# Kernel optimization log

Hardware: AMD Instinct MI355X
Metric: run time of the kernel (lower is better)

The kernel has to match this reference:

```python
import jax, jax.numpy as jnp
import numpy as np

SAMPLING_RATE = 0.5

def setup_inputs() -> dict:
    key = jax.random.key(0)
    k1, k2 = jax.random.split(key)
    token = jax.random.normal(k1, (8, 16, 4, 384), dtype=jnp.float32)
    feature = jax.random.normal(k2, (8, 16, 4, 196, 384), dtype=jnp.float32)
    return {"token": token, "feature": feature}

def reference(token, feature):
    b1, n1, kk1, c = token.shape
    b2, n2, kk2, hw, _ = feature.shape
    N = n1 * kk1  # == n2 * kk2
    tok = token.reshape(b1, N, 1, c)           # [b, N, 1, c]
    feat = feature.reshape(b2, N, hw, c)       # [b, N, hw, c]
    scale = c ** (-0.5)
    # attention scores: [b, N, 1, hw]
    attn = jnp.einsum('bnqc,bnhc->bnqh', tok, feat) * scale
    attn = jax.nn.softmax(attn, axis=-1)
    tk = int(hw * SAMPLING_RATE)
    sel_attn, sel_idx = jax.lax.top_k(attn, tk)          # [b, N, 1, tk]
    sel_attn = sel_attn / jnp.sum(sel_attn, axis=-1, keepdims=True)
    # gather selected features: idx [b, N, tk] -> feat rows [b, N, tk, c]
    idx = sel_idx[:, :, 0, :]                            # [b, N, tk]
    sel_feat = jnp.take_along_axis(feat, idx[..., None], axis=2)  # [b, N, tk, c]
    out = jnp.einsum('bnqt,bntc->bnqc', sel_attn, sel_feat)       # [b, N, 1, c]
    return out.reshape(b1, n1, kk1, c)
```

## Files before the change

### kernel.cpp

```cpp
#include <hip/hip_runtime.h>

#define HW 196
#define C  384
#define TK 98
#define NT 512
#define NWAVE (NT/64)
#define NQUAD ((HW+3)/4)

__global__ __launch_bounds__(NT) void sampling_kernel(
    const float* __restrict__ token,
    const float* __restrict__ feature,
    float* __restrict__ out)
{
    __shared__ float tokLds[C];
    __shared__ float score[HW];
    __shared__ float selW[TK];
    __shared__ int   selIdx[TK];
    __shared__ float wsum[NWAVE];
    __shared__ float part[NWAVE][C];
    __shared__ float s_max, s_winv;

    const int tid  = threadIdx.x;
    const int wave = tid >> 6;
    const int lane = tid & 63;
    const int pair = blockIdx.x;

    const float* tokp  = token   + (size_t)pair * C;
    const float* featp = feature + (size_t)pair * (HW * C);

    for (int i = tid; i < C; i += NT) tokLds[i] = tokp[i];
    __syncthreads();

    const float4* t4 = (const float4*)tokLds;
    float4 tb  = t4[lane];
    float4 tb2 = make_float4(0.f, 0.f, 0.f, 0.f);
    if (lane < 32) tb2 = t4[64 + lane];

    const float scale = 0.05103103630798288f;

    for (int q = wave; q < NQUAD; q += NWAVE) {
        const int rbase = q * 4;
        float4 a[4], b[4];
        #pragma unroll
        for (int j = 0; j < 4; ++j) {
            const float4* f4 = (const float4*)(featp + (rbase + j) * C);
            a[j] = f4[lane];
            if (lane < 32) b[j] = f4[64 + lane];
        }
        #pragma unroll
        for (int j = 0; j < 4; ++j) {
            float p = a[j].x*tb.x + a[j].y*tb.y + a[j].z*tb.z + a[j].w*tb.w;
            if (lane < 32)
                p += b[j].x*tb2.x + b[j].y*tb2.y + b[j].z*tb2.z + b[j].w*tb2.w;
            #pragma unroll
            for (int off = 32; off > 0; off >>= 1)
                p += __shfl_xor(p, off, 64);
            if (lane == 0) score[rbase + j] = p * scale;
        }
    }
    __syncthreads();

    if (wave == 0) {
        float m = -3.4e38f;
        for (int i = lane; i < HW; i += 64) m = fmaxf(m, score[i]);
        #pragma unroll
        for (int off = 32; off > 0; off >>= 1)
            m = fmaxf(m, __shfl_xor(m, off, 64));
        if (lane == 0) s_max = m;
    }
    __syncthreads();

    float w = 0.f;
    if (tid < HW) {
        const float si = score[tid];
        int rank = 0;
        for (int j = 0; j < HW; ++j) {
            const float sj = score[j];
            rank += (int)((sj > si) | ((sj == si) & (j < tid)));
        }
        if (rank < TK) {
            w = __expf(si - s_max);
            selIdx[rank] = tid;
            selW[rank]  = w;
        }
    }
    #pragma unroll
    for (int off = 32; off > 0; off >>= 1) w += __shfl_xor(w, off, 64);
    if (lane == 0) wsum[wave] = w;
    __syncthreads();
    if (tid == 0) {
        float s = 0.f;
        #pragma unroll
        for (int i = 0; i < NWAVE; ++i) s += wsum[i];
        s_winv = 1.f / s;
    }
    __syncthreads();

    float4 acc_a = make_float4(0.f, 0.f, 0.f, 0.f);
    float4 acc_b = make_float4(0.f, 0.f, 0.f, 0.f);
    for (int i = wave; i < TK; i += NWAVE) {
        const int   r   = selIdx[i];
        const float wgt = selW[i];
        const float4* f4 = (const float4*)(featp + (size_t)r * C);
        float4 a = f4[lane];
        acc_a.x += wgt * a.x; acc_a.y += wgt * a.y;
        acc_a.z += wgt * a.z; acc_a.w += wgt * a.w;
        if (lane < 32) {
            float4 b = f4[64 + lane];
            acc_b.x += wgt * b.x; acc_b.y += wgt * b.y;
            acc_b.z += wgt * b.z; acc_b.w += wgt * b.w;
        }
    }
    float4* pw = (float4*)&part[wave][0];
    pw[lane] = acc_a;
    if (lane < 32) pw[64 + lane] = acc_b;
    __syncthreads();

    if (tid < C) {
        float s = 0.f;
        #pragma unroll
        for (int wv = 0; wv < NWAVE; ++wv) s += part[wv][tid];
        out[(size_t)pair * C + tid] = s * s_winv;
    }
}

extern "C" void kernel_launch(void* const* d_in, const int* in_sizes, int n_in,
                              void* d_out, int out_size, void* d_ws, size_t ws_size,
                              hipStream_t stream) {
    const float* token   = (const float*)d_in[0];
    const float* feature = (const float*)d_in[1];
    float* out = (float*)d_out;
    const int pairs = in_sizes[0] / C;
    sampling_kernel<<<pairs, NT, 0, stream>>>(token, feature, out);
}
```

Measured before the change: 41.01 us.

## Split score rows across 4-lane groups and unroll gather loop by four

The score phase now gives each 4-lane group its own feature row, accumulating 24 float4 products per lane, so only two shuffle steps are needed per row instead of a full 64-lane reduction for every row. Token values are read from LDS inside the loop instead of being held in registers. The weighted-gather loop is unrolled by four so more row loads can be in flight at once. Launch bounds now request 4 blocks per CU. In the score phase each lane reads 16-byte chunks strided 64 bytes apart within a row, which is less contiguous per load instruction than before, and unrolling plus the occupancy hint may raise register pressure.

```diff
diff --git a/kernel.cpp b/kernel.cpp
--- a/kernel.cpp
+++ b/kernel.cpp
@@ -2,12 +2,12 @@
 
 #define HW 196
 #define C  384
+#define CF4 (C/4)
 #define TK 98
 #define NT 512
 #define NWAVE (NT/64)
-#define NQUAD ((HW+3)/4)
 
-__global__ __launch_bounds__(NT) void sampling_kernel(
+__global__ __launch_bounds__(NT, 4) void sampling_kernel(
     const float* __restrict__ token,
     const float* __restrict__ feature,
     float* __restrict__ out)
@@ -23,39 +23,37 @@
     const int tid  = threadIdx.x;
     const int wave = tid >> 6;
     const int lane = tid & 63;
+    const int g    = lane >> 2;
+    const int l    = lane & 3;
     const int pair = blockIdx.x;
 
     const float* tokp  = token   + (size_t)pair * C;
     const float* featp = feature + (size_t)pair * (HW * C);
+    const float4* f4base = (const float4*)featp;
+    const float4* t4     = (const float4*)tokLds;
 
     for (int i = tid; i < C; i += NT) tokLds[i] = tokp[i];
     __syncthreads();
 
-    const float4* t4 = (const float4*)tokLds;
-    float4 tb  = t4[lane];
-    float4 tb2 = make_float4(0.f, 0.f, 0.f, 0.f);
-    if (lane < 32) tb2 = t4[64 + lane];
-
     const float scale = 0.05103103630798288f;
 
-    for (int q = wave; q < NQUAD; q += NWAVE) {
-        const int rbase = q * 4;
-        float4 a[4], b[4];
-        #pragma unroll
-        for (int j = 0; j < 4; ++j) {
-            const float4* f4 = (const float4*)(featp + (rbase + j) * C);
-            a[j] = f4[lane];
-            if (lane < 32) b[j] = f4[64 + lane];
-        }
-        #pragma unroll
-        for (int j = 0; j < 4; ++j) {
-            float p = a[j].x*tb.x + a[j].y*tb.y + a[j].z*tb.z + a[j].w*tb.w;
-            if (lane < 32)
-                p += b[j].x*tb2.x + b[j].y*tb2.y + b[j].z*tb2.z + b[j].w*tb2.w;
+    #pragma unroll
+    for (int strip = 0; strip < 2; ++strip) {
+        const int r = strip * 128 + wave * 16 + g;
+        if (r < HW) {
+            const float4* f4 = f4base + (size_t)r * CF4;
+            float4 acc = make_float4(0.f, 0.f, 0.f, 0.f);
             #pragma unroll
-            for (int off = 32; off > 0; off >>= 1)
-                p += __shfl_xor(p, off, 64);
-            if (lane == 0) score[rbase + j] = p * scale;
+            for (int k = 0; k < 24; ++k) {
+                float4 a = f4[l + 4 * k];
+                float4 t = t4[l + 4 * k];
+                acc.x += a.x * t.x; acc.y += a.y * t.y;
+                acc.z += a.z * t.z; acc.w += a.w * t.w;
+            }
+            float s = (acc.x + acc.y) + (acc.z + acc.w);
+            s += __shfl_xor(s, 1, 64);
+            s += __shfl_xor(s, 2, 64);
+            if (l == 0) score[r] = s * scale;
         }
     }
     __syncthreads();
@@ -98,17 +96,23 @@
 
     float4 acc_a = make_float4(0.f, 0.f, 0.f, 0.f);
     float4 acc_b = make_float4(0.f, 0.f, 0.f, 0.f);
-    for (int i = wave; i < TK; i += NWAVE) {
-        const int   r   = selIdx[i];
-        const float wgt = selW[i];
-        const float4* f4 = (const float4*)(featp + (size_t)r * C);
-        float4 a = f4[lane];
-        acc_a.x += wgt * a.x; acc_a.y += wgt * a.y;
-        acc_a.z += wgt * a.z; acc_a.w += wgt * a.w;
-        if (lane < 32) {
-            float4 b = f4[64 + lane];
-            acc_b.x += wgt * b.x; acc_b.y += wgt * b.y;
-            acc_b.z += wgt * b.z; acc_b.w += wgt * b.w;
+    for (int base = wave; base < TK; base += 4 * NWAVE) {
+        #pragma unroll
+        for (int j = 0; j < 4; ++j) {
+            const int i = base + j * NWAVE;
+            if (i < TK) {
+                const int   r   = selIdx[i];
+                const float wgt = selW[i];
+                const float4* f4 = f4base + (size_t)r * CF4;
+                float4 a = f4[lane];
+                acc_a.x += wgt * a.x; acc_a.y += wgt * a.y;
+                acc_a.z += wgt * a.z; acc_a.w += wgt * a.w;
+                if (lane < 32) {
+                    float4 b = f4[64 + lane];
+                    acc_b.x += wgt * b.x; acc_b.y += wgt * b.y;
+                    acc_b.z += wgt * b.z; acc_b.w += wgt * b.w;
+                }
+            }
         }
     }
     float4* pw = (float4*)&part[wave][0];
```

New measurement: 39.14 us. 1.05x faster.
